# Performance work log

Hardware: AMD Instinct MI355X
Metric: run time of the kernel (lower is better)

## Reference

```python
import jax, jax.numpy as jnp
import numpy as np

B, S, N, C, D = 1, 6, 10000, 128, 4
HEADS, PTS = 4, 8
HF, WF = 28, 50
M = HF * WF


def setup_inputs() -> dict:
    key0 = jax.random.key(0)
    ks = jax.random.split(key0, 14)
    sc = C ** -0.5
    d = {}
    d["query"] = jax.random.normal(ks[0], (B, N, C), jnp.float32)
    d["key"] = jax.random.normal(ks[1], (S, M, B, C), jnp.float32)
    d["value"] = jax.random.normal(ks[2], (S, M, B, C), jnp.float32)
    d["query_pos"] = jax.random.normal(ks[3], (B, N, C), jnp.float32) * 0.1
    d["reference_points_cam"] = jax.random.uniform(ks[4], (S, B, N, D, 2), jnp.float32, -0.2, 1.2)
    d["bev_mask"] = jax.random.randint(ks[5], (S, B, N, D), 0, 2).astype(bool)
    d["w_off"] = jax.random.normal(ks[6], (C, HEADS * PTS * 2), jnp.float32) * sc
    d["b_off"] = jax.random.normal(ks[7], (HEADS * PTS * 2,), jnp.float32) * 0.01
    d["w_attn"] = jax.random.normal(ks[8], (C, HEADS * PTS), jnp.float32) * sc
    d["b_attn"] = jax.random.normal(ks[9], (HEADS * PTS,), jnp.float32) * 0.01
    d["w_val"] = jax.random.normal(ks[10], (C, C), jnp.float32) * sc
    d["b_val"] = jax.random.normal(ks[11], (C,), jnp.float32) * 0.01
    d["w_out"] = jax.random.normal(ks[12], (C, C), jnp.float32) * sc
    d["b_out"] = jax.random.normal(ks[13], (C,), jnp.float32) * 0.01
    d["Hf"] = HF
    d["Wf"] = WF
    return d


def reference(query, key, value, query_pos, reference_points_cam, bev_mask,
              w_off, b_off, w_attn, b_attn, w_val, b_val, w_out, b_out, Hf, Wf):
    # SpatialCrossAttention with MSDeformAttn3D (BEVFormer semantics, eval mode: dropout=identity).
    # The torch data-dependent gather/rebatch/scatter is replaced by mathematically equivalent
    # masked computation: deformable attention is per-query independent, so running it for all
    # BEV queries per camera and mask-accumulating yields identical slots.
    B_, N_, C_ = query.shape
    S_ = key.shape[0]
    D_ = reference_points_cam.shape[3]
    H, P = HEADS, PTS
    dh = C_ // H
    Pd = P // D_
    q = query + query_pos  # (B,N,C)
    off = (q @ w_off + b_off).reshape(B_, N_, H, Pd, D_, 2)
    aw = jax.nn.softmax((q @ w_attn + b_attn).reshape(B_, N_, H, P), axis=-1)  # over levels*points (L=1)
    # value projection; per-camera feature maps laid out as (B,S,H,Hf*Wf,dh)
    v = jnp.transpose(value, (2, 0, 1, 3))  # (B,S,M,C)
    v = v @ w_val + b_val
    v = v.reshape(B_, S_, Hf * Wf, H, dh).transpose(0, 1, 3, 2, 4)  # (B,S,H,M,dh)
    ref = jnp.transpose(reference_points_cam, (1, 0, 2, 3, 4))  # (B,S,N,D,2)
    norm = jnp.array([Wf, Hf], jnp.float32)  # offset_normalizer = (W, H)
    loc = ref[:, :, :, None, None, :, :] + off[:, None] / norm  # (B,S,N,H,Pd,D,2)
    loc = loc.reshape(B_, S_, N_, H, P, 2)
    # bilinear sampling, zero padding, align_corners=False
    ix = loc[..., 0] * Wf - 0.5
    iy = loc[..., 1] * Hf - 0.5
    x0 = jnp.floor(ix)
    y0 = jnp.floor(iy)

    def flat(a):  # (B,S,N,H,P) -> (B,S,H,N*P)
        return a.transpose(0, 1, 3, 2, 4).reshape(B_, S_, H, N_ * P)

    def gather(xi, yi):
        ok = (xi >= 0) & (xi < Wf) & (yi >= 0) & (yi < Hf)
        xi_c = jnp.clip(xi, 0, Wf - 1).astype(jnp.int32)
        yi_c = jnp.clip(yi, 0, Hf - 1).astype(jnp.int32)
        idx = flat(yi_c * Wf + xi_c)
        g = jnp.take_along_axis(v, idx[..., None], axis=3)  # (B,S,H,N*P,dh)
        return g * flat(ok.astype(v.dtype))[..., None]

    wx1 = ix - x0
    wy1 = iy - y0
    wx0 = 1.0 - wx1
    wy0 = 1.0 - wy1
    samp = (gather(x0, y0) * flat(wx0 * wy0)[..., None]
            + gather(x0 + 1, y0) * flat(wx1 * wy0)[..., None]
            + gather(x0, y0 + 1) * flat(wx0 * wy1)[..., None]
            + gather(x0 + 1, y0 + 1) * flat(wx1 * wy1)[..., None])  # (B,S,H,N*P,dh)
    samp = samp.reshape(B_, S_, H, N_, P, dh)
    out = jnp.einsum('bshnpd,bnhp->bsnhd', samp, aw).reshape(B_, S_, N_, C_)
    # masked scatter-accumulate back to BEV slots
    mask = jnp.transpose(jnp.any(bev_mask, axis=-1), (1, 0, 2))  # (B,S,N)
    slots = jnp.sum(out * mask[..., None].astype(out.dtype), axis=1)  # (B,N,C)
    count = jnp.maximum(mask.astype(out.dtype).sum(axis=1), 1.0)
    slots = slots / count[..., None]
    return slots @ w_out + b_out + query  # dropout is identity in eval
```

## Files before the change

### kernel.cpp

```cpp
#include <hip/hip_runtime.h>
#include <math.h>

#define S_ 6
#define N_ 10000
#define C_ 128
#define D_ 4
#define H_ 4
#define P_ 8
#define HF_ 28
#define WF_ 50
#define M_ (HF_ * WF_)
#define DH_ 32
#define SM_ (S_ * M_)
#define ABYTES (S_ * H_ * M_ * 32)
#define VB_SH (M_ * 32)
#define NSH (S_ * H_)
#define CQ 256
#define NCH ((N_ + CQ - 1) / CQ)

#define NB_V ((SM_ + 31) / 32)
#define NB_O ((N_ + 31) / 32)

typedef float floatx2 __attribute__((ext_vector_type(2)));
typedef _Float16 half2h __attribute__((ext_vector_type(2)));

template <int NC, int MT, int MR, int MODE>
__device__ __forceinline__ void gemm_body(
    const float* __restrict__ A, const float* __restrict__ A2,
    const float* __restrict__ B0, const float* __restrict__ B1,
    const float* __restrict__ bias0, const float* __restrict__ bias1,
    float* __restrict__ outf, char* __restrict__ out8,
    int Mrows, int m0, int tid, int nthreads, float (*Alds)[132]) {
  constexpr int NTHR = (NC / 4) * (MT / MR);

  for (int i = tid; i < MT * 32; i += nthreads) {
    int r = i >> 5, k = (i & 31) * 4;
    int row = m0 + r;
    float4 v = make_float4(0.f, 0.f, 0.f, 0.f);
    if (row < Mrows) {
      v = *(const float4*)(A + (size_t)row * C_ + k);
      if (MODE == 1) {
        float4 v2 = *(const float4*)(A2 + (size_t)row * C_ + k);
        v.x += v2.x; v.y += v2.y; v.z += v2.z; v.w += v2.w;
      }
    }
    *(float4*)(&Alds[r][k]) = v;
  }
  __syncthreads();
  if (tid >= NTHR) return;

  int ci = tid % (NC / 4);
  int mi = tid / (NC / 4);
  int c0 = ci * 4, r0 = mi * MR;

  const float* bs;
  if (MODE == 1) bs = (c0 < 64) ? bias0 + c0 : bias1 + (c0 - 64);
  else bs = bias0 + c0;

  float acc[MR][4];
#pragma unroll
  for (int j = 0; j < MR; ++j)
#pragma unroll
    for (int cc = 0; cc < 4; ++cc) acc[j][cc] = bs[cc];

#pragma unroll 2
  for (int k4 = 0; k4 < C_; k4 += 4) {
    float bf[16];
#pragma unroll
    for (int kk = 0; kk < 4; ++kk) {
      int k = k4 + kk;
      float4 b4;
      if (MODE == 1)
        b4 = (c0 < 64) ? *(const float4*)(B0 + (size_t)k * 64 + c0)
                       : *(const float4*)(B1 + (size_t)k * 32 + (c0 - 64));
      else
        b4 = *(const float4*)(B0 + (size_t)k * NC + c0);
      bf[kk * 4 + 0] = b4.x; bf[kk * 4 + 1] = b4.y;
      bf[kk * 4 + 2] = b4.z; bf[kk * 4 + 3] = b4.w;
    }
    float af[MR * 4];
#pragma unroll
    for (int j = 0; j < MR; ++j) {
      float4 a4 = *(const float4*)(&Alds[r0 + j][k4]);
      af[j * 4 + 0] = a4.x; af[j * 4 + 1] = a4.y;
      af[j * 4 + 2] = a4.z; af[j * 4 + 3] = a4.w;
    }
#pragma unroll
    for (int j = 0; j < MR; ++j)
#pragma unroll
      for (int kk = 0; kk < 4; ++kk)
#pragma unroll
        for (int cc = 0; cc < 4; ++cc)
          acc[j][cc] = fmaf(af[j * 4 + kk], bf[kk * 4 + cc], acc[j][cc]);
  }

#pragma unroll
  for (int j = 0; j < MR; ++j) {
    int row = m0 + r0 + j;
    if (row >= Mrows) continue;
    if (MODE == 0) {
      int mm = row % M_;
      int h = c0 >> 5, d0 = c0 & 31;
      int s = row / M_;
      int w = __builtin_amdgcn_cvt_pk_fp8_f32(acc[j][0], acc[j][1], 0, false);
      w = __builtin_amdgcn_cvt_pk_fp8_f32(acc[j][2], acc[j][3], w, true);
      size_t hm = (size_t)s * H_ + h;
      *(int*)(out8 + (hm * M_ + mm) * 32 + d0) = w;
    } else if (MODE == 1) {
      *(float4*)(outf + (size_t)row * 96 + c0) =
          make_float4(acc[j][0], acc[j][1], acc[j][2], acc[j][3]);
    }
  }
}

__global__ __launch_bounds__(256) void prep_kernel(
    const float* __restrict__ value, const float* __restrict__ w_val,
    const float* __restrict__ b_val, char* __restrict__ vh8,
    const float* __restrict__ query, const float* __restrict__ query_pos,
    const float* __restrict__ w_off, const float* __restrict__ b_off,
    const float* __restrict__ w_attn, const float* __restrict__ b_attn,
    float* __restrict__ OFFL) {
  __shared__ float Alds[32][132];
  int bid = blockIdx.x;
  if (bid < NB_V) {
    gemm_body<128, 32, 4, 0>(value, nullptr, w_val, nullptr, b_val, nullptr,
                             nullptr, vh8, SM_, bid * 32, threadIdx.x, 256,
                             Alds);
  } else {
    gemm_body<96, 32, 4, 1>(query, query_pos, w_off, w_attn, b_off, b_attn,
                            OFFL, nullptr, N_, (bid - NB_V) * 32, threadIdx.x,
                            256, Alds);
  }
}

__global__ __launch_bounds__(256, 2) void attn3_kernel(
    const float* __restrict__ OFFL,
    const float* __restrict__ refpts,
    const int*   __restrict__ bev_mask,
    const char*  __restrict__ wsbase,
    float* __restrict__ part) {
  __shared__ int4 Vl4[VB_SH / 16];
  __shared__ int4 Pp[CQ * 9];

  int bid = blockIdx.x;
  int sh = bid % NSH;
  int q0 = (bid / NSH) * CQ;
  int s = sh >> 2, h = sh & 3;
  int tid = threadIdx.x;

  const int4* vsrc = (const int4*)(wsbase + 64 + (size_t)sh * VB_SH);
#pragma unroll 4
  for (int i = tid; i < VB_SH / 16; i += 256) Vl4[i] = vsrc[i];

  {
    int q = q0 + tid;
    float aw[8], rx[4], ry[4];
    int sm = 0;
    if (q < N_) {
      const float* lg = OFFL + (size_t)q * 96 + 64 + h * 8;
      float mx = -1e30f;
#pragma unroll
      for (int p = 0; p < 8; ++p) mx = fmaxf(mx, lg[p]);
      float sum = 0.f;
#pragma unroll
      for (int p = 0; p < 8; ++p) { aw[p] = expf(lg[p] - mx); sum += aw[p]; }
      float is = 1.f / sum;
#pragma unroll
      for (int p = 0; p < 8; ++p) aw[p] *= is;
      const int* bm = bev_mask + ((size_t)s * N_ + q) * D_;
      sm = (bm[0] | bm[1] | bm[2] | bm[3]) ? 1 : 0;
      const float* rf = refpts + ((size_t)s * N_ + q) * 8;
#pragma unroll
      for (int dd = 0; dd < 4; ++dd) {
        rx[dd] = rf[dd * 2 + 0];
        ry[dd] = rf[dd * 2 + 1];
      }
    }
#pragma unroll
    for (int p = 0; p < 8; ++p) {
      int4 pk = {0, 0, 0, 0};
      if (q < N_) {
        int pd = p >> 2, dd = p & 3;
        float ox = OFFL[(size_t)q * 96 + h * 16 + pd * 8 + dd * 2 + 0];
        float oy = OFFL[(size_t)q * 96 + h * 16 + pd * 8 + dd * 2 + 1];
        float ix = rx[dd] * (float)WF_ + ox - 0.5f;
        float iy = ry[dd] * (float)HF_ + oy - 0.5f;
        float xf = floorf(ix), yf = floorf(iy);
        int x0 = (int)xf, y0 = (int)yf;
        float wx1 = ix - xf, wy1 = iy - yf;
        float wx0 = 1.f - wx1, wy0 = 1.f - wy1;
        float a = aw[p] * (float)sm;
        bool vx0 = (x0 >= 0) && (x0 < WF_);
        bool vx1 = (x0 + 1 >= 0) && (x0 + 1 < WF_);
        bool vy0 = (y0 >= 0) && (y0 < HF_);
        bool vy1 = (y0 + 1 >= 0) && (y0 + 1 < HF_);
        float w00 = (vx0 && vy0) ? wx0 * wy0 * a : 0.f;
        float w10 = (vx1 && vy0) ? wx1 * wy0 * a : 0.f;
        float w01 = (vx0 && vy1) ? wx0 * wy1 * a : 0.f;
        float w11 = (vx1 && vy1) ? wx1 * wy1 * a : 0.f;
        int yt = min(max(y0, 0), HF_ - 1) * WF_;
        int yb = min(max(y0 + 1, 0), HF_ - 1) * WF_;
        int xc0 = min(max(x0, 0), WF_ - 1);
        int xc1 = min(max(x0 + 1, 0), WF_ - 1);
        pk.x = yt | (yb << 16);
        pk.y = xc0 | (xc1 << 16);
        union { half2h hv; int iv; } u01, u23;
        u01.hv = (half2h){(_Float16)w00, (_Float16)w10};
        u23.hv = (half2h){(_Float16)w01, (_Float16)w11};
        pk.z = u01.iv;
        pk.w = u23.iv;
      }
      Pp[tid * 9 + p] = pk;
    }
  }
  __syncthreads();

  {
    int w = tid >> 6, lane = tid & 63;
    int qg = lane >> 3, c8 = lane & 7;
    int rowsel = (c8 >> 2) & 1, xsel = (c8 >> 1) & 1, chalf = c8 & 1;
    int role = c8 >> 1;
    int rsh = rowsel << 4, xsh = xsel << 4, wsh = (role & 1) << 4;

    for (int pass = 0; pass < CQ / 32; ++pass) {
      int ql = pass * 32 + w * 8 + qg;
      int q = q0 + ql;
      const int4* pp = &Pp[ql * 9];
      floatx2 acc[8] = {{0.f, 0.f}, {0.f, 0.f}, {0.f, 0.f}, {0.f, 0.f},
                        {0.f, 0.f}, {0.f, 0.f}, {0.f, 0.f}, {0.f, 0.f}};
#pragma unroll
      for (int p = 0; p < 8; ++p) {
        int4 prm = pp[p];
        int yoff = (prm.x >> rsh) & 0xffff;
        int xoff = (prm.y >> xsh) & 0xffff;
        int vidx = (yoff + xoff) * 2 + chalf;
        unsigned wz = (unsigned)((role & 2) ? prm.w : prm.z);
        union { unsigned short u; _Float16 hf; } cu;
        cu.u = (unsigned short)((wz >> wsh) & 0xffffu);
        float wgt = (float)cu.hf;
        floatx2 wv = {wgt, wgt};
        int4 tv = Vl4[vidx];
        acc[0] += __builtin_amdgcn_cvt_pk_f32_fp8(tv.x, false) * wv;
        acc[1] += __builtin_amdgcn_cvt_pk_f32_fp8(tv.x, true)  * wv;
        acc[2] += __builtin_amdgcn_cvt_pk_f32_fp8(tv.y, false) * wv;
        acc[3] += __builtin_amdgcn_cvt_pk_f32_fp8(tv.y, true)  * wv;
        acc[4] += __builtin_amdgcn_cvt_pk_f32_fp8(tv.z, false) * wv;
        acc[5] += __builtin_amdgcn_cvt_pk_f32_fp8(tv.z, true)  * wv;
        acc[6] += __builtin_amdgcn_cvt_pk_f32_fp8(tv.w, false) * wv;
        acc[7] += __builtin_amdgcn_cvt_pk_f32_fp8(tv.w, true)  * wv;
      }
      float av[16];
#pragma unroll
      for (int k = 0; k < 8; ++k) {
        av[2 * k] = acc[k][0];
        av[2 * k + 1] = acc[k][1];
      }
#pragma unroll
      for (int k = 0; k < 16; ++k) av[k] += __shfl_xor(av[k], 2);
#pragma unroll
      for (int k = 0; k < 16; ++k) av[k] += __shfl_xor(av[k], 4);
      if (c8 < 2 && q < N_) {
        float* dst = part + ((size_t)sh * N_ + q) * 32 + chalf * 16;
        *(float4*)(dst + 0)  = make_float4(av[0], av[1], av[2], av[3]);
        *(float4*)(dst + 4)  = make_float4(av[4], av[5], av[6], av[7]);
        *(float4*)(dst + 8)  = make_float4(av[8], av[9], av[10], av[11]);
        *(float4*)(dst + 12) = make_float4(av[12], av[13], av[14], av[15]);
      }
    }
  }
}

__global__ __launch_bounds__(256) void reduce_kernel(
    const float* __restrict__ part, const int* __restrict__ bev_mask,
    const float* __restrict__ query, const float* __restrict__ w_out,
    const float* __restrict__ b_out, float* __restrict__ out) {
  __shared__ float slds[32][132];
  __shared__ float sinv[32];
  int q0 = blockIdx.x * 32, tid = threadIdx.x;

  if (tid < 32) {
    int q = q0 + tid, cnt = 0;
    if (q < N_) {
#pragma unroll
      for (int s = 0; s < S_; ++s) {
        const int* bm = bev_mask + ((size_t)s * N_ + q) * D_;
        cnt += (bm[0] | bm[1] | bm[2] | bm[3]) ? 1 : 0;
      }
    }
    sinv[tid] = 1.f / (float)(cnt > 0 ? cnt : 1);
  }
  __syncthreads();

  {
    int ql = tid >> 3, c16 = (tid & 7) * 16;
    int q = q0 + ql, h = c16 >> 5, d0 = c16 & 31;
    float a[16];
#pragma unroll
    for (int k = 0; k < 16; ++k) a[k] = 0.f;
    if (q < N_) {
#pragma unroll
      for (int s = 0; s < S_; ++s) {
        const float* src = part + ((size_t)(s * H_ + h) * N_ + q) * 32 + d0;
#pragma unroll
        for (int k = 0; k < 16; k += 4) {
          float4 v = *(const float4*)(src + k);
          a[k + 0] += v.x; a[k + 1] += v.y; a[k + 2] += v.z; a[k + 3] += v.w;
        }
      }
    }
    float inv = sinv[ql];
    float* dst = &slds[ql][c16];
#pragma unroll
    for (int k = 0; k < 16; k += 4)
      *(float4*)(dst + k) =
          make_float4(a[k] * inv, a[k + 1] * inv, a[k + 2] * inv, a[k + 3] * inv);
  }
  __syncthreads();

  {
    int ci = tid & 31, mi = tid >> 5;
    int c0 = ci * 4, r0 = mi * 4;
    float acc[4][4];
#pragma unroll
    for (int j = 0; j < 4; ++j) {
      int q = q0 + r0 + j;
      int qq = (q < N_) ? q : (N_ - 1);
      float4 qv = *(const float4*)(query + (size_t)qq * C_ + c0);
      float4 bv = *(const float4*)(b_out + c0);
      acc[j][0] = bv.x + qv.x; acc[j][1] = bv.y + qv.y;
      acc[j][2] = bv.z + qv.z; acc[j][3] = bv.w + qv.w;
    }
#pragma unroll 2
    for (int k4 = 0; k4 < C_; k4 += 4) {
      float bf[16];
#pragma unroll
      for (int kk = 0; kk < 4; ++kk) {
        float4 b4 = *(const float4*)(w_out + (size_t)(k4 + kk) * C_ + c0);
        bf[kk * 4 + 0] = b4.x; bf[kk * 4 + 1] = b4.y;
        bf[kk * 4 + 2] = b4.z; bf[kk * 4 + 3] = b4.w;
      }
      float af[16];
#pragma unroll
      for (int j = 0; j < 4; ++j) {
        float4 a4 = *(const float4*)(&slds[r0 + j][k4]);
        af[j * 4 + 0] = a4.x; af[j * 4 + 1] = a4.y;
        af[j * 4 + 2] = a4.z; af[j * 4 + 3] = a4.w;
      }
#pragma unroll
      for (int j = 0; j < 4; ++j)
#pragma unroll
        for (int kk = 0; kk < 4; ++kk)
#pragma unroll
          for (int cc = 0; cc < 4; ++cc)
            acc[j][cc] = fmaf(af[j * 4 + kk], bf[kk * 4 + cc], acc[j][cc]);
    }
#pragma unroll
    for (int j = 0; j < 4; ++j) {
      int q = q0 + r0 + j;
      if (q < N_)
        *(float4*)(out + (size_t)q * C_ + c0) =
            make_float4(acc[j][0], acc[j][1], acc[j][2], acc[j][3]);
    }
  }
}

extern "C" void kernel_launch(void* const* d_in, const int* in_sizes, int n_in,
                              void* d_out, int out_size, void* d_ws, size_t ws_size,
                              hipStream_t stream) {
  const float* query     = (const float*)d_in[0];
  const float* value     = (const float*)d_in[2];
  const float* query_pos = (const float*)d_in[3];
  const float* refpts    = (const float*)d_in[4];
  const int*   bev_mask  = (const int*)d_in[5];
  const float* w_off     = (const float*)d_in[6];
  const float* b_off     = (const float*)d_in[7];
  const float* w_attn    = (const float*)d_in[8];
  const float* b_attn    = (const float*)d_in[9];
  const float* w_val     = (const float*)d_in[10];
  const float* b_val     = (const float*)d_in[11];
  const float* w_out     = (const float*)d_in[12];
  const float* b_out     = (const float*)d_in[13];

  char* ws = (char*)d_ws;
  char* vh8   = ws + 64;
  float* OFFL = (float*)(ws + 64 + 2 * (size_t)ABYTES + 64);
  float* PART = (float*)(ws + 64 + 2 * (size_t)ABYTES + 64 +
                         (size_t)N_ * 96 * 4);

  prep_kernel<<<NB_V + NB_O, 256, 0, stream>>>(
      value, w_val, b_val, vh8, query, query_pos, w_off, b_off, w_attn, b_attn,
      OFFL);
  attn3_kernel<<<NSH * NCH, 256, 0, stream>>>(OFFL, refpts, bev_mask, ws,
                                              PART);
  reduce_kernel<<<(N_ + 31) / 32, 256, 0, stream>>>(PART, bev_mask, query,
                                                    w_out, b_out,
                                                    (float*)d_out);
}
```

Measured before the change: 165.6 us.

## Accumulate cameras inside attention kernel, drop partial buffer and reduce pass

The attention kernel now loops over all six cameras per (query chunk, head) block and accumulates the masked, count-normalized slot directly, writing one slot tensor instead of per-camera partials. Each lane computes its own bilinear corner weight in registers rather than staging packed parameters in shared memory. The reduce kernel becomes a plain output projection. This removes the large partial-sum write and read, but the feature map is reloaded into LDS once per camera with extra barriers, and chunks are smaller (64 queries, 512 threads), which may expose that load latency.

```diff
diff --git a/kernel.cpp b/kernel.cpp
--- a/kernel.cpp
+++ b/kernel.cpp
@@ -14,15 +14,13 @@
 #define SM_ (S_ * M_)
 #define ABYTES (S_ * H_ * M_ * 32)
 #define VB_SH (M_ * 32)
-#define NSH (S_ * H_)
-#define CQ 256
+#define CQ 64
 #define NCH ((N_ + CQ - 1) / CQ)
 
 #define NB_V ((SM_ + 31) / 32)
 #define NB_O ((N_ + 31) / 32)
 
 typedef float floatx2 __attribute__((ext_vector_type(2)));
-typedef _Float16 half2h __attribute__((ext_vector_type(2)));
 
 template <int NC, int MT, int MR, int MODE>
 __device__ __forceinline__ void gemm_body(
@@ -133,187 +131,134 @@
   }
 }
 
-__global__ __launch_bounds__(256, 2) void attn3_kernel(
+__global__ __launch_bounds__(512, 2) void attn4_kernel(
     const float* __restrict__ OFFL,
     const float* __restrict__ refpts,
     const int*   __restrict__ bev_mask,
     const char*  __restrict__ wsbase,
-    float* __restrict__ part) {
-  __shared__ int4 Vl4[VB_SH / 16];
-  __shared__ int4 Pp[CQ * 9];
+    float* __restrict__ slot) {
+  __shared__ int4 Vl4[M_ * 2];
 
   int bid = blockIdx.x;
-  int sh = bid % NSH;
-  int q0 = (bid / NSH) * CQ;
-  int s = sh >> 2, h = sh & 3;
+  int h = bid & 3;
+  int q0 = (bid >> 2) * CQ;
   int tid = threadIdx.x;
-
-  const int4* vsrc = (const int4*)(wsbase + 64 + (size_t)sh * VB_SH);
-#pragma unroll 4
-  for (int i = tid; i < VB_SH / 16; i += 256) Vl4[i] = vsrc[i];
-
+  int w = tid >> 6, lane = tid & 63;
+  int qg = lane >> 3, c8 = lane & 7;
+  int rowsel = (c8 >> 2) & 1, xsel = (c8 >> 1) & 1, chalf = c8 & 1;
+
+  int q = q0 + w * 8 + qg;
+  int qvalid = (q < N_);
+  int qc = qvalid ? q : (N_ - 1);
+
+  float off[16];
   {
-    int q = q0 + tid;
-    float aw[8], rx[4], ry[4];
-    int sm = 0;
-    if (q < N_) {
-      const float* lg = OFFL + (size_t)q * 96 + 64 + h * 8;
-      float mx = -1e30f;
-#pragma unroll
-      for (int p = 0; p < 8; ++p) mx = fmaxf(mx, lg[p]);
-      float sum = 0.f;
-#pragma unroll
-      for (int p = 0; p < 8; ++p) { aw[p] = expf(lg[p] - mx); sum += aw[p]; }
-      float is = 1.f / sum;
-#pragma unroll
-      for (int p = 0; p < 8; ++p) aw[p] *= is;
-      const int* bm = bev_mask + ((size_t)s * N_ + q) * D_;
-      sm = (bm[0] | bm[1] | bm[2] | bm[3]) ? 1 : 0;
-      const float* rf = refpts + ((size_t)s * N_ + q) * 8;
-#pragma unroll
-      for (int dd = 0; dd < 4; ++dd) {
-        rx[dd] = rf[dd * 2 + 0];
-        ry[dd] = rf[dd * 2 + 1];
-      }
-    }
+    const float* ob = OFFL + (size_t)qc * 96 + h * 16;
+#pragma unroll
+    for (int i = 0; i < 16; i += 4) {
+      float4 t = *(const float4*)(ob + i);
+      off[i] = t.x; off[i + 1] = t.y; off[i + 2] = t.z; off[i + 3] = t.w;
+    }
+  }
+  float aw[8];
+  {
+    const float* lg = OFFL + (size_t)qc * 96 + 64 + h * 8;
+    float mx = -1e30f;
+#pragma unroll
+    for (int p = 0; p < 8; ++p) { aw[p] = lg[p]; mx = fmaxf(mx, aw[p]); }
+    float sum = 0.f;
+#pragma unroll
+    for (int p = 0; p < 8; ++p) { aw[p] = expf(aw[p] - mx); sum += aw[p]; }
+    float is = 1.f / sum;
+#pragma unroll
+    for (int p = 0; p < 8; ++p) aw[p] *= is;
+  }
+
+  floatx2 acc[8] = {{0.f, 0.f}, {0.f, 0.f}, {0.f, 0.f}, {0.f, 0.f},
+                    {0.f, 0.f}, {0.f, 0.f}, {0.f, 0.f}, {0.f, 0.f}};
+  int cnt = 0;
+
+  for (int s = 0; s < S_; ++s) {
+    __syncthreads();
+    {
+      const int4* vsrc =
+          (const int4*)(wsbase + 64 + (size_t)(s * H_ + h) * VB_SH);
+      for (int i = tid; i < M_ * 2; i += 512) Vl4[i] = vsrc[i];
+    }
+    __syncthreads();
+
+    const int* bm = bev_mask + ((size_t)s * N_ + qc) * D_;
+    int4 bmv = *(const int4*)bm;
+    int sm = (bmv.x | bmv.y | bmv.z | bmv.w) ? 1 : 0;
+    cnt += sm;
+    float smf = (float)sm;
+    float rxy[8];
+    {
+      const float* rf = refpts + ((size_t)s * N_ + qc) * 8;
+      float4 r0 = *(const float4*)(rf + 0);
+      float4 r1 = *(const float4*)(rf + 4);
+      rxy[0] = r0.x; rxy[1] = r0.y; rxy[2] = r0.z; rxy[3] = r0.w;
+      rxy[4] = r1.x; rxy[5] = r1.y; rxy[6] = r1.z; rxy[7] = r1.w;
+    }
+
 #pragma unroll
     for (int p = 0; p < 8; ++p) {
-      int4 pk = {0, 0, 0, 0};
-      if (q < N_) {
-        int pd = p >> 2, dd = p & 3;
-        float ox = OFFL[(size_t)q * 96 + h * 16 + pd * 8 + dd * 2 + 0];
-        float oy = OFFL[(size_t)q * 96 + h * 16 + pd * 8 + dd * 2 + 1];
-        float ix = rx[dd] * (float)WF_ + ox - 0.5f;
-        float iy = ry[dd] * (float)HF_ + oy - 0.5f;
-        float xf = floorf(ix), yf = floorf(iy);
-        int x0 = (int)xf, y0 = (int)yf;
-        float wx1 = ix - xf, wy1 = iy - yf;
-        float wx0 = 1.f - wx1, wy0 = 1.f - wy1;
-        float a = aw[p] * (float)sm;
-        bool vx0 = (x0 >= 0) && (x0 < WF_);
-        bool vx1 = (x0 + 1 >= 0) && (x0 + 1 < WF_);
-        bool vy0 = (y0 >= 0) && (y0 < HF_);
-        bool vy1 = (y0 + 1 >= 0) && (y0 + 1 < HF_);
-        float w00 = (vx0 && vy0) ? wx0 * wy0 * a : 0.f;
-        float w10 = (vx1 && vy0) ? wx1 * wy0 * a : 0.f;
-        float w01 = (vx0 && vy1) ? wx0 * wy1 * a : 0.f;
-        float w11 = (vx1 && vy1) ? wx1 * wy1 * a : 0.f;
-        int yt = min(max(y0, 0), HF_ - 1) * WF_;
-        int yb = min(max(y0 + 1, 0), HF_ - 1) * WF_;
-        int xc0 = min(max(x0, 0), WF_ - 1);
-        int xc1 = min(max(x0 + 1, 0), WF_ - 1);
-        pk.x = yt | (yb << 16);
-        pk.y = xc0 | (xc1 << 16);
-        union { half2h hv; int iv; } u01, u23;
-        u01.hv = (half2h){(_Float16)w00, (_Float16)w10};
-        u23.hv = (half2h){(_Float16)w01, (_Float16)w11};
-        pk.z = u01.iv;
-        pk.w = u23.iv;
-      }
-      Pp[tid * 9 + p] = pk;
-    }
-  }
-  __syncthreads();
-
-  {
-    int w = tid >> 6, lane = tid & 63;
-    int qg = lane >> 3, c8 = lane & 7;
-    int rowsel = (c8 >> 2) & 1, xsel = (c8 >> 1) & 1, chalf = c8 & 1;
-    int role = c8 >> 1;
-    int rsh = rowsel << 4, xsh = xsel << 4, wsh = (role & 1) << 4;
-
-    for (int pass = 0; pass < CQ / 32; ++pass) {
-      int ql = pass * 32 + w * 8 + qg;
-      int q = q0 + ql;
-      const int4* pp = &Pp[ql * 9];
-      floatx2 acc[8] = {{0.f, 0.f}, {0.f, 0.f}, {0.f, 0.f}, {0.f, 0.f},
-                        {0.f, 0.f}, {0.f, 0.f}, {0.f, 0.f}, {0.f, 0.f}};
-#pragma unroll
-      for (int p = 0; p < 8; ++p) {
-        int4 prm = pp[p];
-        int yoff = (prm.x >> rsh) & 0xffff;
-        int xoff = (prm.y >> xsh) & 0xffff;
-        int vidx = (yoff + xoff) * 2 + chalf;
-        unsigned wz = (unsigned)((role & 2) ? prm.w : prm.z);
-        union { unsigned short u; _Float16 hf; } cu;
-        cu.u = (unsigned short)((wz >> wsh) & 0xffffu);
-        float wgt = (float)cu.hf;
-        floatx2 wv = {wgt, wgt};
-        int4 tv = Vl4[vidx];
-        acc[0] += __builtin_amdgcn_cvt_pk_f32_fp8(tv.x, false) * wv;
-        acc[1] += __builtin_amdgcn_cvt_pk_f32_fp8(tv.x, true)  * wv;
-        acc[2] += __builtin_amdgcn_cvt_pk_f32_fp8(tv.y, false) * wv;
-        acc[3] += __builtin_amdgcn_cvt_pk_f32_fp8(tv.y, true)  * wv;
-        acc[4] += __builtin_amdgcn_cvt_pk_f32_fp8(tv.z, false) * wv;
-        acc[5] += __builtin_amdgcn_cvt_pk_f32_fp8(tv.z, true)  * wv;
-        acc[6] += __builtin_amdgcn_cvt_pk_f32_fp8(tv.w, false) * wv;
-        acc[7] += __builtin_amdgcn_cvt_pk_f32_fp8(tv.w, true)  * wv;
-      }
-      float av[16];
-#pragma unroll
-      for (int k = 0; k < 8; ++k) {
-        av[2 * k] = acc[k][0];
-        av[2 * k + 1] = acc[k][1];
-      }
-#pragma unroll
-      for (int k = 0; k < 16; ++k) av[k] += __shfl_xor(av[k], 2);
-#pragma unroll
-      for (int k = 0; k < 16; ++k) av[k] += __shfl_xor(av[k], 4);
-      if (c8 < 2 && q < N_) {
-        float* dst = part + ((size_t)sh * N_ + q) * 32 + chalf * 16;
-        *(float4*)(dst + 0)  = make_float4(av[0], av[1], av[2], av[3]);
-        *(float4*)(dst + 4)  = make_float4(av[4], av[5], av[6], av[7]);
-        *(float4*)(dst + 8)  = make_float4(av[8], av[9], av[10], av[11]);
-        *(float4*)(dst + 12) = make_float4(av[12], av[13], av[14], av[15]);
-      }
-    }
-  }
-}
-
-__global__ __launch_bounds__(256) void reduce_kernel(
-    const float* __restrict__ part, const int* __restrict__ bev_mask,
-    const float* __restrict__ query, const float* __restrict__ w_out,
-    const float* __restrict__ b_out, float* __restrict__ out) {
+      int dd = p & 3;
+      float ix = rxy[dd * 2 + 0] * (float)WF_ + off[2 * p + 0] - 0.5f;
+      float iy = rxy[dd * 2 + 1] * (float)HF_ + off[2 * p + 1] - 0.5f;
+      float xf = floorf(ix), yf = floorf(iy);
+      int x0 = (int)xf, y0 = (int)yf;
+      float fx = ix - xf, fy = iy - yf;
+      float wx = xsel ? fx : (1.f - fx);
+      float wy = rowsel ? fy : (1.f - fy);
+      int xs = x0 + xsel, ys = y0 + rowsel;
+      bool ok = (xs >= 0) & (xs < WF_) & (ys >= 0) & (ys < HF_);
+      float wgt = ok ? wx * wy * aw[p] * smf : 0.f;
+      int xc = min(max(xs, 0), WF_ - 1);
+      int yc = min(max(ys, 0), HF_ - 1);
+      int vidx = (yc * WF_ + xc) * 2 + chalf;
+      int4 tv = Vl4[vidx];
+      floatx2 wv = {wgt, wgt};
+      acc[0] += __builtin_amdgcn_cvt_pk_f32_fp8(tv.x, false) * wv;
+      acc[1] += __builtin_amdgcn_cvt_pk_f32_fp8(tv.x, true)  * wv;
+      acc[2] += __builtin_amdgcn_cvt_pk_f32_fp8(tv.y, false) * wv;
+      acc[3] += __builtin_amdgcn_cvt_pk_f32_fp8(tv.y, true)  * wv;
+      acc[4] += __builtin_amdgcn_cvt_pk_f32_fp8(tv.z, false) * wv;
+      acc[5] += __builtin_amdgcn_cvt_pk_f32_fp8(tv.z, true)  * wv;
+      acc[6] += __builtin_amdgcn_cvt_pk_f32_fp8(tv.w, false) * wv;
+      acc[7] += __builtin_amdgcn_cvt_pk_f32_fp8(tv.w, true)  * wv;
+    }
+  }
+
+  float av[16];
+#pragma unroll
+  for (int k = 0; k < 8; ++k) { av[2 * k] = acc[k][0]; av[2 * k + 1] = acc[k][1]; }
+#pragma unroll
+  for (int k = 0; k < 16; ++k) av[k] += __shfl_xor(av[k], 2);
+#pragma unroll
+  for (int k = 0; k < 16; ++k) av[k] += __shfl_xor(av[k], 4);
+
+  float inv = 1.f / (float)(cnt > 0 ? cnt : 1);
+  if (c8 < 2 && qvalid) {
+    float* dst = slot + (size_t)q * C_ + h * DH_ + chalf * 16;
+    *(float4*)(dst + 0)  = make_float4(av[0] * inv, av[1] * inv, av[2] * inv, av[3] * inv);
+    *(float4*)(dst + 4)  = make_float4(av[4] * inv, av[5] * inv, av[6] * inv, av[7] * inv);
+    *(float4*)(dst + 8)  = make_float4(av[8] * inv, av[9] * inv, av[10] * inv, av[11] * inv);
+    *(float4*)(dst + 12) = make_float4(av[12] * inv, av[13] * inv, av[14] * inv, av[15] * inv);
+  }
+}
+
+__global__ __launch_bounds__(256) void outproj_kernel(
+    const float* __restrict__ slot, const float* __restrict__ query,
+    const float* __restrict__ w_out, const float* __restrict__ b_out,
+    float* __restrict__ out) {
   __shared__ float slds[32][132];
-  __shared__ float sinv[32];
   int q0 = blockIdx.x * 32, tid = threadIdx.x;
 
-  if (tid < 32) {
-    int q = q0 + tid, cnt = 0;
-    if (q < N_) {
-#pragma unroll
-      for (int s = 0; s < S_; ++s) {
-        const int* bm = bev_mask + ((size_t)s * N_ + q) * D_;
-        cnt += (bm[0] | bm[1] | bm[2] | bm[3]) ? 1 : 0;
-      }
-    }
-    sinv[tid] = 1.f / (float)(cnt > 0 ? cnt : 1);
-  }
-  __syncthreads();
-
-  {
-    int ql = tid >> 3, c16 = (tid & 7) * 16;
-    int q = q0 + ql, h = c16 >> 5, d0 = c16 & 31;
-    float a[16];
-#pragma unroll
-    for (int k = 0; k < 16; ++k) a[k] = 0.f;
-    if (q < N_) {
-#pragma unroll
-      for (int s = 0; s < S_; ++s) {
-        const float* src = part + ((size_t)(s * H_ + h) * N_ + q) * 32 + d0;
-#pragma unroll
-        for (int k = 0; k < 16; k += 4) {
-          float4 v = *(const float4*)(src + k);
-          a[k + 0] += v.x; a[k + 1] += v.y; a[k + 2] += v.z; a[k + 3] += v.w;
-        }
-      }
-    }
-    float inv = sinv[ql];
-    float* dst = &slds[ql][c16];
-#pragma unroll
-    for (int k = 0; k < 16; k += 4)
-      *(float4*)(dst + k) =
-          make_float4(a[k] * inv, a[k + 1] * inv, a[k + 2] * inv, a[k + 3] * inv);
+  for (int i = tid; i < 32 * 32; i += 256) {
+    int r = i >> 5, k = (i & 31) * 4;
+    int qc = min(q0 + r, N_ - 1);
+    *(float4*)(&slds[r][k]) = *(const float4*)(slot + (size_t)qc * C_ + k);
   }
   __syncthreads();
 
@@ -323,8 +268,7 @@
     float acc[4][4];
 #pragma unroll
     for (int j = 0; j < 4; ++j) {
-      int q = q0 + r0 + j;
-      int qq = (q < N_) ? q : (N_ - 1);
+      int qq = min(q0 + r0 + j, N_ - 1);
       float4 qv = *(const float4*)(query + (size_t)qq * C_ + c0);
       float4 bv = *(const float4*)(b_out + c0);
       acc[j][0] = bv.x + qv.x; acc[j][1] = bv.y + qv.y;
@@ -356,9 +300,9 @@
     }
 #pragma unroll
     for (int j = 0; j < 4; ++j) {
-      int q = q0 + r0 + j;
-      if (q < N_)
-        *(float4*)(out + (size_t)q * C_ + c0) =
+      int qq = q0 + r0 + j;
+      if (qq < N_)
+        *(float4*)(out + (size_t)qq * C_ + c0) =
             make_float4(acc[j][0], acc[j][1], acc[j][2], acc[j][3]);
     }
   }
@@ -384,15 +328,13 @@
   char* ws = (char*)d_ws;
   char* vh8   = ws + 64;
   float* OFFL = (float*)(ws + 64 + 2 * (size_t)ABYTES + 64);
-  float* PART = (float*)(ws + 64 + 2 * (size_t)ABYTES + 64 +
+  float* SLOT = (float*)(ws + 64 + 2 * (size_t)ABYTES + 64 +
                          (size_t)N_ * 96 * 4);
 
   prep_kernel<<<NB_V + NB_O, 256, 0, stream>>>(
       value, w_val, b_val, vh8, query, query_pos, w_off, b_off, w_attn, b_attn,
       OFFL);
-  attn3_kernel<<<NSH * NCH, 256, 0, stream>>>(OFFL, refpts, bev_mask, ws,
-                                              PART);
-  reduce_kernel<<<(N_ + 31) / 32, 256, 0, stream>>>(PART, bev_mask, query,
-                                                    w_out, b_out,
-                                                    (float*)d_out);
-}
+  attn4_kernel<<<NCH * H_, 512, 0, stream>>>(OFFL, refpts, bev_mask, ws, SLOT);
+  outproj_kernel<<<(N_ + 31) / 32, 256, 0, stream>>>(SLOT, query, w_out, b_out,
+                                                     (float*)d_out);
+}
```

Result: no change. 167.5 us (+1.1%).
